# Performance work log

Hardware: AMD Instinct MI355X
Metric: run time of the kernel (lower is better)

The kernel has to match this reference:

```python
import jax, jax.numpy as jnp
import numpy as np

N_NODES = 100000
IN_DIM = 128
HID_DIM = 128
N_EDGES = 1600000
BN_EPS = 1e-5


def setup_inputs() -> dict:
    key = jax.random.key(0)
    k1, k2, k3, k4 = jax.random.split(key, 4)
    x = jax.random.normal(k1, (N_NODES, IN_DIM), dtype=jnp.float32)
    edge_index = jax.random.randint(k2, (2, N_EDGES), 0, N_NODES, dtype=jnp.int64)
    # GCNConv linear weight (glorot) and bias
    W = jax.random.normal(k3, (HID_DIM, IN_DIM), dtype=jnp.float32) * (1.0 / np.sqrt(IN_DIM))
    b = jnp.zeros((HID_DIM,), dtype=jnp.float32)
    # BatchNorm affine params
    gamma = jnp.ones((HID_DIM,), dtype=jnp.float32)
    beta = jnp.zeros((HID_DIM,), dtype=jnp.float32)
    return {"x": x, "edge_index": edge_index, "W": W, "b": b, "gamma": gamma, "beta": beta}


def reference(x, edge_index, W, b, gamma, beta):
    n = x.shape[0]
    # --- GCNConv: add self loops, symmetric normalization ---
    loops = jnp.arange(n, dtype=edge_index.dtype)
    row = jnp.concatenate([edge_index[0], loops])  # source j
    col = jnp.concatenate([edge_index[1], loops])  # target i
    deg = jax.ops.segment_sum(jnp.ones_like(col, dtype=x.dtype), col, num_segments=n)
    deg_inv_sqrt = jnp.where(deg > 0, jax.lax.rsqrt(jnp.maximum(deg, 1e-12)), 0.0)
    norm = deg_inv_sqrt[row] * deg_inv_sqrt[col]  # [E+N]
    # linear transform then normalized gather-scatter aggregation
    h = x @ W.T  # [N, H]
    msgs = h[row] * norm[:, None]  # [E+N, H]
    out = jax.ops.segment_sum(msgs, col, num_segments=n) + b  # [N, H]
    # --- BatchNorm1d (training-mode batch stats, biased var) + ReLU ---
    mean = jnp.mean(out, axis=0)
    var = jnp.mean(jnp.square(out - mean), axis=0)
    out = (out - mean) * jax.lax.rsqrt(var + BN_EPS) * gamma + beta
    return jax.nn.relu(out)
```

## Files before the change

kernel.cpp:

```cpp
#include <hip/hip_runtime.h>

#define N_NODES 100000
#define N_EDGES 1600000
#define BN_EPS 1e-5f
#define SB 25
#define SCAP 69632
#define NBB 800
#define CAP 2688

typedef short short8 __attribute__((ext_vector_type(8)));
typedef float floatx4 __attribute__((ext_vector_type(4)));

__device__ __forceinline__ unsigned short f2bf(float f) {
    unsigned int u = __float_as_uint(f);
    unsigned int r = (u + 0x7fffu + ((u >> 16) & 1u)) >> 16;
    return (unsigned short)r;
}
__device__ __forceinline__ float bflo(unsigned int v) { return __uint_as_float(v << 16); }
__device__ __forceinline__ float bfhi(unsigned int v) { return __uint_as_float(v & 0xffff0000u); }

__global__ __launch_bounds__(512) void k_binA(const int* __restrict__ ei,
                                              int* __restrict__ scnt,
                                              unsigned int* __restrict__ b1, int E) {
    __shared__ int hist[32], base[32], gbase[32];
    __shared__ unsigned int stage[4096];
    __shared__ unsigned char stb[4096];
    int tid = threadIdx.x;
    int e0 = blockIdx.x * 4096;
    int cn = min(4096, E - e0);
    if (tid < 32) hist[tid] = 0;
    __syncthreads();

    unsigned int mycode[8];
    short myslot[8];
    signed char myb[8];
    #pragma unroll
    for (int j = 0; j < 8; j++) {
        int idx = j * 512 + tid;
        if (idx < cn) {
            int src = ei[e0 + idx];
            int dst = ei[E + e0 + idx];
            int s = dst >> 12;
            mycode[j] = (unsigned int)src | ((unsigned int)(dst & 4095) << 17);
            myb[j] = (signed char)s;
            myslot[j] = (short)atomicAdd(&hist[s], 1);
        } else myb[j] = -1;
    }
    __syncthreads();
    if (tid == 0) {
        int run = 0;
        for (int s = 0; s < SB; s++) { base[s] = run; run += hist[s]; }
    }
    __syncthreads();
    #pragma unroll
    for (int j = 0; j < 8; j++) {
        if (myb[j] >= 0) {
            int p = base[myb[j]] + myslot[j];
            stage[p] = mycode[j];
            stb[p] = (unsigned char)myb[j];
        }
    }
    if (tid < SB && hist[tid]) gbase[tid] = tid * SCAP + atomicAdd(&scnt[tid], hist[tid]);
    __syncthreads();
    for (int i = tid; i < cn; i += 512) {
        int s = stb[i];
        b1[gbase[s] + (i - base[s])] = stage[i];
    }
}

__global__ __launch_bounds__(512) void k_binB(const unsigned int* __restrict__ b1,
                                              const int* __restrict__ scnt,
                                              int* __restrict__ bcnt,
                                              unsigned int* __restrict__ b2) {
    __shared__ int hist[32], base[32], gbase[32];
    __shared__ unsigned int stage[4096];
    __shared__ unsigned char stb[4096];
    int tid = threadIdx.x;
    int s = blockIdx.x / 17;
    int c = blockIdx.x % 17;
    int cnt = scnt[s];
    int e0 = s * SCAP + c * 4096;
    int cn = min(4096, cnt - c * 4096);
    if (tid < 32) hist[tid] = 0;
    __syncthreads();

    unsigned int mycode[8];
    short myslot[8];
    signed char myb[8];
    #pragma unroll
    for (int j = 0; j < 8; j++) {
        int idx = j * 512 + tid;
        if (idx < cn) {
            unsigned int code = b1[e0 + idx];
            int sub = (code >> 24) & 31;
            mycode[j] = code & 0x00FFFFFFu;
            myb[j] = (signed char)sub;
            myslot[j] = (short)atomicAdd(&hist[sub], 1);
        } else myb[j] = -1;
    }
    __syncthreads();
    if (tid == 0) {
        int run = 0;
        for (int k = 0; k < 32; k++) { base[k] = run; run += hist[k]; }
    }
    __syncthreads();
    #pragma unroll
    for (int j = 0; j < 8; j++) {
        if (myb[j] >= 0) {
            int p = base[myb[j]] + myslot[j];
            stage[p] = mycode[j];
            stb[p] = (unsigned char)myb[j];
        }
    }
    if (tid < 32 && hist[tid]) {
        int gb = s * 32 + tid;
        gbase[tid] = gb * CAP + atomicAdd(&bcnt[gb], hist[tid]);
    }
    __syncthreads();
    for (int i = tid; i < cn; i += 512) {
        int sub = stb[i];
        b2[gbase[sub] + (i - base[sub])] = stage[i];
    }
}

__global__ __launch_bounds__(256) void k_sortd(unsigned int* __restrict__ b2,
        const int* __restrict__ bcnt, int* __restrict__ offs, int* __restrict__ deg,
        float* __restrict__ dinv, int n) {
    __shared__ unsigned int stage[CAP];
    __shared__ int hist[128], hsc[128];
    int b = blockIdx.x, t = threadIdx.x;
    int nb0 = b * 128;
    int e0 = b * CAP;
    int cnt = bcnt[b];
    if (t < 128) hist[t] = 0;
    __syncthreads();
    for (int i = t; i < cnt; i += 256) {
        unsigned int code = b2[e0 + i];
        stage[i] = code;
        atomicAdd(&hist[code >> 17], 1);
    }
    __syncthreads();
    int v = (t < 128) ? hist[t] : 0;
    if (t < 128) hsc[t] = v;
    __syncthreads();
    for (int o = 1; o < 128; o <<= 1) {
        int x = (t < 128 && t >= o) ? hsc[t - o] : 0;
        __syncthreads();
        if (t < 128) hsc[t] += x;
        __syncthreads();
    }
    int nr = min(128, n - nb0);
    if (t < nr) {
        int start = hsc[t] - v;
        offs[nb0 + t] = start;
        deg[nb0 + t] = v;
        dinv[nb0 + t] = rsqrtf((float)(v + 1));
        hist[t] = start;
    }
    __syncthreads();
    for (int i = t; i < cnt; i += 256) {
        unsigned int code = stage[i];
        int pos = atomicAdd(&hist[code >> 17], 1);
        b2[e0 + pos] = code & 0x1FFFF;
    }
}

__global__ void k_wcvt(const float* __restrict__ Wf, unsigned short* __restrict__ Wb) {
    int i = blockIdx.x * 256 + threadIdx.x;
    if (i < 128 * 128) Wb[i] = f2bf(Wf[i]);
}

__global__ __launch_bounds__(256) void k_gemm(const float* __restrict__ x,
                                              const unsigned short* __restrict__ Wb,
                                              const float* __restrict__ dinv,
                                              unsigned short* __restrict__ gb, int n) {
    int w = threadIdx.x >> 6;
    int l = threadIdx.x & 63;
    int rowbase = blockIdx.x * 128 + w * 32;
    int r16 = l & 15;
    int kg = l >> 4;

    short8 a[2][4];
    float dv[2][4];
    #pragma unroll
    for (int m = 0; m < 2; m++) {
        int row = rowbase + m * 16 + r16;
        int rca = min(row, n - 1);
        const float* base = x + rca * 128;
        #pragma unroll
        for (int q = 0; q < 4; q++) {
            const float4* xp = (const float4*)(base + q * 32 + kg * 8);
            float4 lo = xp[0], hi = xp[1];
            short8 af;
            af[0] = (short)f2bf(lo.x); af[1] = (short)f2bf(lo.y);
            af[2] = (short)f2bf(lo.z); af[3] = (short)f2bf(lo.w);
            af[4] = (short)f2bf(hi.x); af[5] = (short)f2bf(hi.y);
            af[6] = (short)f2bf(hi.z); af[7] = (short)f2bf(hi.w);
            a[m][q] = af;
        }
        #pragma unroll
        for (int r = 0; r < 4; r++)
            dv[m][r] = dinv[min(rowbase + m * 16 + kg * 4 + r, n - 1)];
    }
    for (int t = 0; t < 8; t++) {
        int col = t * 16 + r16;
        short8 b[4];
        #pragma unroll
        for (int q = 0; q < 4; q++)
            b[q] = *(const short8*)(Wb + col * 128 + q * 32 + kg * 8);

        floatx4 acc[2] = {};
        #pragma unroll
        for (int m = 0; m < 2; m++)
            #pragma unroll
            for (int q = 0; q < 4; q++)
                acc[m] = __builtin_amdgcn_mfma_f32_16x16x32_bf16(a[m][q], b[q], acc[m], 0, 0, 0);

        #pragma unroll
        for (int m = 0; m < 2; m++) {
            #pragma unroll
            for (int r = 0; r < 4; r++) {
                int row = rowbase + m * 16 + kg * 4 + r;
                if (row < n) gb[row * 128 + col] = f2bf(acc[m][r] * dv[m][r]);
            }
        }
    }
}

__global__ __launch_bounds__(512) void k_fused2(const unsigned int* __restrict__ hp,
        const float* __restrict__ dinv, const int* __restrict__ bcnt,
        const int* __restrict__ offs, const int* __restrict__ deg,
        const unsigned int* __restrict__ b2, float* __restrict__ out,
        float* __restrict__ sums, float* __restrict__ sumsq, int n) {
    __shared__ unsigned int sh_src[CAP];
    __shared__ float dl[128];
    __shared__ int loff[128], ldeg[128];
    __shared__ float ps[8][64], pq[8][64];
    int t = threadIdx.x;
    int w = t >> 6, l = t & 63;
    int bid = blockIdx.x;
    int b = bid >> 1;
    int ch = bid & 1;
    int half = l >> 5;
    int cu = ch * 32 + (l & 31);
    int nb0 = b * 128;
    int e0 = b * CAP;
    int cnt = bcnt[b];
    int nr = min(128, n - nb0);

    if (t < 128 && t < nr) {
        dl[t] = dinv[nb0 + t];
        loff[t] = offs[nb0 + t];
        ldeg[t] = deg[nb0 + t];
    }
    for (int i = t; i < cnt; i += 512) sh_src[i] = b2[e0 + i];
    __syncthreads();

    float s0 = 0, s1 = 0, q0 = 0, q1 = 0;
    for (int r = w; r < nr; r += 8) {
        int i = nb0 + r;
        float di = dl[r];
        float ax = 0.f, ay = 0.f;
        int off = loff[r];
        int dg = ldeg[r];
        int e = 0;
        for (; e + 15 < dg; e += 16) {
            unsigned int hv[8];
            #pragma unroll
            for (int j = 0; j < 8; j++)
                hv[j] = hp[sh_src[off + e + 2 * j + half] * 64 + cu];
            #pragma unroll
            for (int j = 0; j < 8; j++) {
                ax += bflo(hv[j]);
                ay += bfhi(hv[j]);
            }
        }
        for (; e + 3 < dg; e += 4) {
            unsigned int h0 = hp[sh_src[off + e + half] * 64 + cu];
            unsigned int h1 = hp[sh_src[off + e + 2 + half] * 64 + cu];
            ax += bflo(h0) + bflo(h1);
            ay += bfhi(h0) + bfhi(h1);
        }
        for (; e < dg; e += 2) {
            int idx = e + half;
            if (idx < dg) {
                unsigned int hv = hp[sh_src[off + idx] * 64 + cu];
                ax += bflo(hv);
                ay += bfhi(hv);
            }
        }
        ax += __shfl_xor(ax, 32);
        ay += __shfl_xor(ay, 32);
        if (half == 0) {
            unsigned int sv = hp[i * 64 + cu];
            float v0 = di * (ax + bflo(sv));
            float v1 = di * (ay + bfhi(sv));
            ((float2*)out)[i * 64 + cu] = make_float2(v0, v1);
            s0 += v0; q0 += v0 * v0;
            s1 += v1; q1 += v1 * v1;
        }
    }

    if (half == 0) {
        ps[w][2 * (l & 31)] = s0; ps[w][2 * (l & 31) + 1] = s1;
        pq[w][2 * (l & 31)] = q0; pq[w][2 * (l & 31) + 1] = q1;
    }
    __syncthreads();
    if (t < 64) {
        float s = 0, q = 0;
        #pragma unroll
        for (int j = 0; j < 8; j++) { s += ps[j][t]; q += pq[j][t]; }
        atomicAdd(&sums[ch * 64 + t], s);
        atomicAdd(&sumsq[ch * 64 + t], q);
    }
}

__global__ void k_bn(float* __restrict__ out, const float* __restrict__ sums,
                     const float* __restrict__ sumsq, const float* __restrict__ gamma,
                     const float* __restrict__ beta, int n) {
    int idx = blockIdx.x * 256 + threadIdx.x;
    int total = n * 32;
    if (idx >= total) return;
    int c0 = (idx & 31) * 4;
    float invN = 1.0f / (float)n;
    float4 v = ((const float4*)out)[idx];
    float r[4] = {v.x, v.y, v.z, v.w};
    #pragma unroll
    for (int j = 0; j < 4; j++) {
        int c = c0 + j;
        float mean = sums[c] * invN;
        float var = sumsq[c] * invN - mean * mean;
        float scale = rsqrtf(var + BN_EPS) * gamma[c];
        float o = (r[j] - mean) * scale + beta[c];
        r[j] = fmaxf(o, 0.0f);
    }
    ((float4*)out)[idx] = make_float4(r[0], r[1], r[2], r[3]);
}

extern "C" void kernel_launch(void* const* d_in, const int* in_sizes, int n_in,
                              void* d_out, int out_size, void* d_ws, size_t ws_size,
                              hipStream_t stream) {
    const float* x     = (const float*)d_in[0];
    const int*   ei    = (const int*)d_in[1];
    const float* W     = (const float*)d_in[2];
    const float* gamma = (const float*)d_in[4];
    const float* beta  = (const float*)d_in[5];
    float* out = (float*)d_out;

    const int n = N_NODES, E = N_EDGES;

    unsigned short* gbuf = (unsigned short*)d_ws;
    float* dinv   = (float*)(gbuf + 12800000);
    int*   offs   = (int*)(dinv + 100000);
    int*   deg    = offs + 100000;
    float* sums   = (float*)(deg + 100000);
    float* sumsq  = sums + 128;
    int*   bcnt   = (int*)(sumsq + 128);
    int*   scnt   = bcnt + NBB;
    unsigned short* Wb = (unsigned short*)(scnt + SB);
    unsigned int* b1 = (unsigned int*)(Wb + 16384);
    unsigned int* b2 = b1 + SB * SCAP;

    hipMemsetAsync(sums, 0, (256 + NBB + SB) * sizeof(int), stream);

    k_binA<<<(E + 4095) / 4096, 512, 0, stream>>>(ei, scnt, b1, E);
    k_binB<<<SB * 17, 512, 0, stream>>>(b1, scnt, bcnt, b2);
    k_sortd<<<NBB, 256, 0, stream>>>(b2, bcnt, offs, deg, dinv, n);

    k_wcvt<<<64, 256, 0, stream>>>(W, Wb);
    k_gemm<<<(n + 127) / 128, 256, 0, stream>>>(x, Wb, dinv, gbuf, n);

    k_fused2<<<NBB * 2, 512, 0, stream>>>((const unsigned int*)gbuf, dinv, bcnt, offs, deg,
                                          (const unsigned int*)b2, out, sums, sumsq, n);

    k_bn<<<(n * 32 + 255) / 256, 256, 0, stream>>>(out, sums, sumsq, gamma, beta, n);
}
```

Baseline: 167.6 us.

## Widen gather loads to uint2 and interleave two rows per warp

```diff
diff --git a/kernel.cpp b/kernel.cpp
--- a/kernel.cpp
+++ b/kernel.cpp
@@ -227,7 +227,23 @@
     }
 }
 
-__global__ __launch_bounds__(512) void k_fused2(const unsigned int* __restrict__ hp,
+__device__ __forceinline__ void load4u2(const uint2* __restrict__ hp2,
+        const unsigned int* __restrict__ sh_src, int off, int e, int qt, int cu2,
+        uint2 v[4]) {
+    #pragma unroll
+    for (int j = 0; j < 4; j++)
+        v[j] = hp2[(int)sh_src[off + e + 4 * j + qt] * 32 + cu2];
+}
+__device__ __forceinline__ void acc4u2(const uint2 v[4], float& a0, float& a1,
+                                       float& a2, float& a3) {
+    #pragma unroll
+    for (int j = 0; j < 4; j++) {
+        a0 += bflo(v[j].x); a1 += bfhi(v[j].x);
+        a2 += bflo(v[j].y); a3 += bfhi(v[j].y);
+    }
+}
+
+__global__ __launch_bounds__(512, 8) void k_fused2(const uint2* __restrict__ hp2,
         const float* __restrict__ dinv, const int* __restrict__ bcnt,
         const int* __restrict__ offs, const int* __restrict__ deg,
         const unsigned int* __restrict__ b2, float* __restrict__ out,
@@ -241,8 +257,9 @@
     int bid = blockIdx.x;
     int b = bid >> 1;
     int ch = bid & 1;
-    int half = l >> 5;
-    int cu = ch * 32 + (l & 31);
+    int qt = l >> 4;
+    int m = l & 15;
+    int cu2 = ch * 16 + m;
     int nb0 = b * 128;
     int e0 = b * CAP;
     int cnt = bcnt[b];
@@ -256,62 +273,102 @@
     for (int i = t; i < cnt; i += 512) sh_src[i] = b2[e0 + i];
     __syncthreads();
 
-    float s0 = 0, s1 = 0, q0 = 0, q1 = 0;
-    for (int r = w; r < nr; r += 8) {
-        int i = nb0 + r;
-        float di = dl[r];
-        float ax = 0.f, ay = 0.f;
-        int off = loff[r];
-        int dg = ldeg[r];
-        int e = 0;
-        for (; e + 15 < dg; e += 16) {
-            unsigned int hv[8];
-            #pragma unroll
-            for (int j = 0; j < 8; j++)
-                hv[j] = hp[sh_src[off + e + 2 * j + half] * 64 + cu];
-            #pragma unroll
-            for (int j = 0; j < 8; j++) {
-                ax += bflo(hv[j]);
-                ay += bfhi(hv[j]);
+    float ss0 = 0, ss1 = 0, ss2 = 0, ss3 = 0;
+    float sq0 = 0, sq1 = 0, sq2 = 0, sq3 = 0;
+    for (int rr = w; rr < nr; rr += 16) {
+        int rA = rr, rB = rr + 8;
+        bool hasB = rB < nr;
+        float diA = dl[rA];
+        int offA = loff[rA], dgA = ldeg[rA];
+        float diB = hasB ? dl[rB] : 0.f;
+        int offB = hasB ? loff[rB] : 0;
+        int dgB = hasB ? ldeg[rB] : 0;
+        float aA0 = 0, aA1 = 0, aA2 = 0, aA3 = 0;
+        float aB0 = 0, aB1 = 0, aB2 = 0, aB3 = 0;
+        int eA = 0, eB = 0;
+        while (eA + 15 < dgA && eB + 15 < dgB) {
+            uint2 va[4], vb[4];
+            load4u2(hp2, sh_src, offA, eA, qt, cu2, va);
+            load4u2(hp2, sh_src, offB, eB, qt, cu2, vb);
+            acc4u2(va, aA0, aA1, aA2, aA3);
+            acc4u2(vb, aB0, aB1, aB2, aB3);
+            eA += 16; eB += 16;
+        }
+        while (eA + 15 < dgA) {
+            uint2 va[4];
+            load4u2(hp2, sh_src, offA, eA, qt, cu2, va);
+            acc4u2(va, aA0, aA1, aA2, aA3);
+            eA += 16;
+        }
+        while (eB + 15 < dgB) {
+            uint2 vb[4];
+            load4u2(hp2, sh_src, offB, eB, qt, cu2, vb);
+            acc4u2(vb, aB0, aB1, aB2, aB3);
+            eB += 16;
+        }
+        for (; eA < dgA; eA += 8) {
+            int i1 = eA + qt, i2 = eA + 4 + qt;
+            uint2 v1 = make_uint2(0u, 0u), v2 = make_uint2(0u, 0u);
+            if (i1 < dgA) v1 = hp2[(int)sh_src[offA + i1] * 32 + cu2];
+            if (i2 < dgA) v2 = hp2[(int)sh_src[offA + i2] * 32 + cu2];
+            aA0 += bflo(v1.x) + bflo(v2.x); aA1 += bfhi(v1.x) + bfhi(v2.x);
+            aA2 += bflo(v1.y) + bflo(v2.y); aA3 += bfhi(v1.y) + bfhi(v2.y);
+        }
+        for (; eB < dgB; eB += 8) {
+            int i1 = eB + qt, i2 = eB + 4 + qt;
+            uint2 v1 = make_uint2(0u, 0u), v2 = make_uint2(0u, 0u);
+            if (i1 < dgB) v1 = hp2[(int)sh_src[offB + i1] * 32 + cu2];
+            if (i2 < dgB) v2 = hp2[(int)sh_src[offB + i2] * 32 + cu2];
+            aB0 += bflo(v1.x) + bflo(v2.x); aB1 += bfhi(v1.x) + bfhi(v2.x);
+            aB2 += bflo(v1.y) + bflo(v2.y); aB3 += bfhi(v1.y) + bfhi(v2.y);
+        }
+        aA0 += __shfl_xor(aA0, 16); aA0 += __shfl_xor(aA0, 32);
+        aA1 += __shfl_xor(aA1, 16); aA1 += __shfl_xor(aA1, 32);
+        aA2 += __shfl_xor(aA2, 16); aA2 += __shfl_xor(aA2, 32);
+        aA3 += __shfl_xor(aA3, 16); aA3 += __shfl_xor(aA3, 32);
+        aB0 += __shfl_xor(aB0, 16); aB0 += __shfl_xor(aB0, 32);
+        aB1 += __shfl_xor(aB1, 16); aB1 += __shfl_xor(aB1, 32);
+        aB2 += __shfl_xor(aB2, 16); aB2 += __shfl_xor(aB2, 32);
+        aB3 += __shfl_xor(aB3, 16); aB3 += __shfl_xor(aB3, 32);
+        if (qt == 0) {
+            uint2 sv = hp2[(nb0 + rA) * 32 + cu2];
+            float v0 = diA * (aA0 + bflo(sv.x));
+            float v1 = diA * (aA1 + bfhi(sv.x));
+            float v2 = diA * (aA2 + bflo(sv.y));
+            float v3 = diA * (aA3 + bfhi(sv.y));
+            ((float4*)out)[(nb0 + rA) * 32 + cu2] = make_float4(v0, v1, v2, v3);
+            ss0 += v0; sq0 += v0 * v0;
+            ss1 += v1; sq1 += v1 * v1;
+            ss2 += v2; sq2 += v2 * v2;
+            ss3 += v3; sq3 += v3 * v3;
+            if (hasB) {
+                uint2 sb = hp2[(nb0 + rB) * 32 + cu2];
+                float u0 = diB * (aB0 + bflo(sb.x));
+                float u1 = diB * (aB1 + bfhi(sb.x));
+                float u2 = diB * (aB2 + bflo(sb.y));
+                float u3 = diB * (aB3 + bfhi(sb.y));
+                ((float4*)out)[(nb0 + rB) * 32 + cu2] = make_float4(u0, u1, u2, u3);
+                ss0 += u0; sq0 += u0 * u0;
+                ss1 += u1; sq1 += u1 * u1;
+                ss2 += u2; sq2 += u2 * u2;
+                ss3 += u3; sq3 += u3 * u3;
             }
         }
-        for (; e + 3 < dg; e += 4) {
-            unsigned int h0 = hp[sh_src[off + e + half] * 64 + cu];
-            unsigned int h1 = hp[sh_src[off + e + 2 + half] * 64 + cu];
-            ax += bflo(h0) + bflo(h1);
-            ay += bfhi(h0) + bfhi(h1);
-        }
-        for (; e < dg; e += 2) {
-            int idx = e + half;
-            if (idx < dg) {
-                unsigned int hv = hp[sh_src[off + idx] * 64 + cu];
-                ax += bflo(hv);
-                ay += bfhi(hv);
-            }
-        }
-        ax += __shfl_xor(ax, 32);
-        ay += __shfl_xor(ay, 32);
-        if (half == 0) {
-            unsigned int sv = hp[i * 64 + cu];
-            float v0 = di * (ax + bflo(sv));
-            float v1 = di * (ay + bfhi(sv));
-            ((float2*)out)[i * 64 + cu] = make_float2(v0, v1);
-            s0 += v0; q0 += v0 * v0;
-            s1 += v1; q1 += v1 * v1;
-        }
-    }
-
-    if (half == 0) {
-        ps[w][2 * (l & 31)] = s0; ps[w][2 * (l & 31) + 1] = s1;
-        pq[w][2 * (l & 31)] = q0; pq[w][2 * (l & 31) + 1] = q1;
+    }
+
+    if (qt == 0) {
+        ps[w][4 * m + 0] = ss0; ps[w][4 * m + 1] = ss1;
+        ps[w][4 * m + 2] = ss2; ps[w][4 * m + 3] = ss3;
+        pq[w][4 * m + 0] = sq0; pq[w][4 * m + 1] = sq1;
+        pq[w][4 * m + 2] = sq2; pq[w][4 * m + 3] = sq3;
     }
     __syncthreads();
     if (t < 64) {
-        float s = 0, q = 0;
-        #pragma unroll
-        for (int j = 0; j < 8; j++) { s += ps[j][t]; q += pq[j][t]; }
+        float s = 0, qq = 0;
+        #pragma unroll
+        for (int j = 0; j < 8; j++) { s += ps[j][t]; qq += pq[j][t]; }
         atomicAdd(&sums[ch * 64 + t], s);
-        atomicAdd(&sumsq[ch * 64 + t], q);
+        atomicAdd(&sumsq[ch * 64 + t], qq);
     }
 }
 
@@ -370,7 +427,7 @@
     k_wcvt<<<64, 256, 0, stream>>>(W, Wb);
     k_gemm<<<(n + 127) / 128, 256, 0, stream>>>(x, Wb, dinv, gbuf, n);
 
-    k_fused2<<<NBB * 2, 512, 0, stream>>>((const unsigned int*)gbuf, dinv, bcnt, offs, deg,
+    k_fused2<<<NBB * 2, 512, 0, stream>>>((const uint2*)gbuf, dinv, bcnt, offs, deg,
                                           (const unsigned int*)b2, out, sums, sumsq, n);
 
     k_bn<<<(n * 32 + 255) / 256, 256, 0, stream>>>(out, sums, sumsq, gamma, beta, n);
```

Result: faster. 160.9 us (-4.0%).
